# Performance work log

Measured on AMD Instinct MI355X. Metric: run time of the kernel, lower is better.

Reference implementation:

```python
import jax, jax.numpy as jnp
import numpy as np

N_NODES = 100000
N_EDGES = 3200000
F_IN = 128
F_HID = 16
F_OUT = 1


def setup_inputs() -> dict:
    key = jax.random.key(0)
    ks = jax.random.split(key, 8)
    x = jax.random.normal(ks[0], (N_NODES, F_IN), dtype=jnp.float32)
    src = jax.random.randint(ks[1], (N_EDGES,), 0, N_NODES, dtype=jnp.int32)
    dst = jax.random.randint(ks[2], (N_EDGES,), 0, N_NODES, dtype=jnp.int32)
    edge_w = jax.random.uniform(ks[3], (N_EDGES,), dtype=jnp.float32)
    W0 = jax.random.normal(ks[4], (F_IN, F_HID), dtype=jnp.float32) / np.sqrt(F_IN)
    b0 = jnp.zeros((F_HID,), dtype=jnp.float32)
    W1 = jax.random.normal(ks[5], (F_HID, F_OUT), dtype=jnp.float32) / np.sqrt(F_HID)
    b1 = jnp.zeros((F_OUT,), dtype=jnp.float32)
    return {"x": x, "src": src, "dst": dst, "edge_w": edge_w,
            "W0": W0, "b0": b0, "W1": W1, "b1": b1}


def _spmm(src, dst, edge_w, h):
    # sparse A (COO) @ dense h: gather rows at src, weight, scatter-add to dst
    msgs = h[src] * edge_w[:, None]            # [E, F]
    return jax.ops.segment_sum(msgs, dst, num_segments=N_NODES)  # [N, F]


def reference(x, src, dst, edge_w, W0, b0, W1, b1):
    # GCNConv layer 0: relu(A @ (x @ W0) + b0)
    z0 = x @ W0                                 # [N, 16] linear transform first
    h = jax.nn.relu(_spmm(src, dst, edge_w, z0) + b0)
    # (Dropout is identity at inference)
    # GCNConv layer 1: sigmoid(A @ (h @ W1) + b1)
    z1 = h @ W1                                 # [N, 1]
    out = jax.nn.sigmoid(_spmm(src, dst, edge_w, z1) + b1)
    return out
```

## Files before the change

kernel.cpp:

```cpp
#include <hip/hip_runtime.h>

#define N_NODES 100000
#define N_EDGES 3200000
#define F_IN 128
#define F_HID 16

#define BK_LG 7
#define BK_NODES 128
#define NB ((N_NODES + BK_NODES - 1) / BK_NODES)
#define BCAPF 4800
#define CLG 10
#define CNODES 1024
#define NBC ((N_NODES + CNODES - 1) / CNODES)
#define NBC_P 128
#define BCAPC 34816
#define CPB2 9
#define CHUNK 4096
#define BIN_T 512
#define EPT (CHUNK / BIN_T)
#define CUR_STRIDE 16

__device__ __forceinline__ unsigned short f2bf_rne(float f) {
    unsigned u = __float_as_uint(f);
    u += 0x7FFFu + ((u >> 16) & 1u);
    return (unsigned short)(u >> 16);
}

__global__ __launch_bounds__(256) void k_xw0(const float* __restrict__ x,
                                             const float* __restrict__ W0,
                                             unsigned short* __restrict__ z0b, int n) {
    __shared__ float xs[64][F_IN + 1];
    __shared__ float w0s[F_IN * F_HID];
    const int tid = threadIdx.x;
    for (int i = tid; i < F_IN * F_HID; i += 256) w0s[i] = W0[i];
    const int row0 = blockIdx.x * 64;
    for (int i = tid; i < 64 * (F_IN / 4); i += 256) {
        int r  = i / (F_IN / 4);
        int c4 = i % (F_IN / 4);
        float4 v = make_float4(0.f, 0.f, 0.f, 0.f);
        int row = row0 + r;
        if (row < n) v = ((const float4*)(x + (size_t)row * F_IN))[c4];
        xs[r][c4 * 4 + 0] = v.x; xs[r][c4 * 4 + 1] = v.y;
        xs[r][c4 * 4 + 2] = v.z; xs[r][c4 * 4 + 3] = v.w;
    }
    __syncthreads();
    const int r  = tid & 63;
    const int cg = tid >> 6;
    float a0 = 0.f, a1 = 0.f, a2 = 0.f, a3 = 0.f;
    #pragma unroll 8
    for (int k = 0; k < F_IN; ++k) {
        float xv = xs[r][k];
        a0 = fmaf(xv, w0s[k * F_HID + cg * 4 + 0], a0);
        a1 = fmaf(xv, w0s[k * F_HID + cg * 4 + 1], a1);
        a2 = fmaf(xv, w0s[k * F_HID + cg * 4 + 2], a2);
        a3 = fmaf(xv, w0s[k * F_HID + cg * 4 + 3], a3);
    }
    int row = row0 + r;
    if (row < n) {
        ushort4 p = make_ushort4(f2bf_rne(a0), f2bf_rne(a1), f2bf_rne(a2), f2bf_rne(a3));
        *(ushort4*)(z0b + (size_t)row * F_HID + cg * 4) = p;
    }
}

__global__ __launch_bounds__(BIN_T) void k_bin1(const int* __restrict__ src,
                                                const int* __restrict__ dst,
                                                const float* __restrict__ ew,
                                                int* __restrict__ cursorC,
                                                int2* __restrict__ ebinC) {
    __shared__ int cnt[NBC_P], excl[NBC_P], run[NBC_P], gb[NBC_P], alw[NBC_P];
    __shared__ int2 stage[CHUNK];
    __shared__ unsigned char sbid[CHUNK];
    const int tid = threadIdx.x;
    const int e0  = blockIdx.x * CHUNK;
    const int nch = min(CHUNK, N_EDGES - e0);

    for (int i = tid; i < NBC_P; i += BIN_T) cnt[i] = 0;
    __syncthreads();

    int es[EPT], eb[EPT], edl[EPT]; float ww[EPT];
    #pragma unroll
    for (int k = 0; k < EPT; ++k) {
        int idx = k * BIN_T + tid;
        if (idx < nch) {
            int e = e0 + idx;
            int d = dst[e];
            es[k]  = src[e];
            ww[k]  = ew[e];
            eb[k]  = d >> CLG;
            edl[k] = d & (CNODES - 1);
            atomicAdd(&cnt[eb[k]], 1);
        } else {
            eb[k] = -1;
        }
    }
    __syncthreads();

    if (tid < NBC_P) excl[tid] = cnt[tid];
    __syncthreads();
    for (int off = 1; off < NBC_P; off <<= 1) {
        int v = 0;
        if (tid < NBC_P && tid >= off) v = excl[tid - off];
        __syncthreads();
        if (tid < NBC_P && tid >= off) excl[tid] += v;
        __syncthreads();
    }
    if (tid < NBC_P) excl[tid] -= cnt[tid];
    __syncthreads();

    if (tid < NBC) {
        int c = cnt[tid];
        if (c > 0) {
            int old = atomicAdd(&cursorC[tid * CUR_STRIDE], c);
            int a = BCAPC - old;
            a = (a < 0) ? 0 : ((a > c) ? c : a);
            alw[tid] = a;
            gb[tid]  = tid * BCAPC + old;
        } else {
            alw[tid] = 0;
            gb[tid]  = tid * BCAPC;
        }
        run[tid] = 0;
    }
    __syncthreads();

    #pragma unroll
    for (int k = 0; k < EPT; ++k) {
        if (eb[k] >= 0) {
            int b = eb[k];
            int p = excl[b] + atomicAdd(&run[b], 1);
            stage[p] = make_int2(__float_as_int(ww[k]), es[k] | (edl[k] << 17));
            sbid[p]  = (unsigned char)b;
        }
    }
    __syncthreads();

    for (int s = tid; s < nch; s += BIN_T) {
        int b   = sbid[s];
        int off = s - excl[b];
        if (off < alw[b]) ebinC[(size_t)gb[b] + off] = stage[s];
    }
}

__global__ __launch_bounds__(BIN_T) void k_bin2(const int* __restrict__ cursorC,
                                                const int2* __restrict__ ebinC,
                                                int* __restrict__ cursorF,
                                                int2* __restrict__ ebinF) {
    __shared__ int cntw[64], runw[64], base[64];
    __shared__ int totals[8], excl_s[8], gb8[8], alw8[8];
    __shared__ int2 stage[CHUNK];
    __shared__ unsigned char sbid[CHUNK];
    const int tid = threadIdx.x;
    const int wid = tid >> 6;
    const int c   = blockIdx.x / CPB2;
    const int ck  = blockIdx.x % CPB2;
    const int ecnt = min(cursorC[c * CUR_STRIDE], BCAPC);
    const int beg  = ck * CHUNK;
    const int n2   = min(CHUNK, ecnt - beg);
    if (n2 <= 0) return;
    const int2* eC = ebinC + (size_t)c * BCAPC + beg;

    if (tid < 64) { cntw[tid] = 0; runw[tid] = 0; }
    __syncthreads();

    int fid[EPT]; int2 pk[EPT];
    #pragma unroll
    for (int k = 0; k < EPT; ++k) {
        int idx = k * BIN_T + tid;
        if (idx < n2) {
            int2 e = eC[idx];
            int dlc = e.y >> 17;
            int f   = dlc >> BK_LG;
            fid[k]  = f;
            pk[k]   = make_int2(e.x, (e.y & 0x1FFFF) | ((dlc & (BK_NODES - 1)) << 17));
            atomicAdd(&cntw[f * 8 + wid], 1);
        } else {
            fid[k] = -1;
        }
    }
    __syncthreads();

    if (tid < 8) {
        int t = 0;
        #pragma unroll
        for (int w = 0; w < 8; ++w) t += cntw[tid * 8 + w];
        totals[tid] = t;
    }
    __syncthreads();
    if (tid < 8) {
        int e = 0;
        for (int f = 0; f < 8; ++f) if (f < tid) e += totals[f];
        excl_s[tid] = e;
        int t = totals[tid];
        int fb = c * 8 + tid;
        if (t > 0 && fb < NB) {
            int old = atomicAdd(&cursorF[fb * CUR_STRIDE], t);
            int a = BCAPF - old;
            a = (a < 0) ? 0 : ((a > t) ? t : a);
            alw8[tid] = a;
            gb8[tid]  = fb * BCAPF + old;
        } else {
            alw8[tid] = 0;
            gb8[tid]  = 0;
        }
    }
    __syncthreads();
    if (tid < 64) {
        int f = tid >> 3, w = tid & 7;
        int bb = excl_s[f];
        for (int w2 = 0; w2 < 8; ++w2) if (w2 < w) bb += cntw[f * 8 + w2];
        base[tid] = bb;
    }
    __syncthreads();

    #pragma unroll
    for (int k = 0; k < EPT; ++k) {
        if (fid[k] >= 0) {
            int slot = fid[k] * 8 + wid;
            int p = base[slot] + atomicAdd(&runw[slot], 1);
            stage[p] = pk[k];
            sbid[p]  = (unsigned char)fid[k];
        }
    }
    __syncthreads();

    for (int s = tid; s < n2; s += BIN_T) {
        int f   = sbid[s];
        int off = s - excl_s[f];
        if (off < alw8[f]) ebinF[(size_t)gb8[f] + off] = stage[s];
    }
}

__global__ __launch_bounds__(512) void k_sg0(const int* __restrict__ cursorF,
                                             const int2* __restrict__ ebinF,
                                             const unsigned short* __restrict__ z0b,
                                             const float* __restrict__ b0,
                                             const float* __restrict__ W1,
                                             float* __restrict__ z1) {
    __shared__ int2 stage[BCAPF];
    __shared__ unsigned short idx[BCAPF];
    __shared__ int hist[BK_NODES], scn[BK_NODES], run[BK_NODES];
    __shared__ float b0s[16], w1s[16];
    const int tid  = threadIdx.x;
    const int lane = tid & 63, wid = tid >> 6;
    const int b    = blockIdx.x;
    if (tid < 16)       { b0s[tid] = b0[tid]; w1s[tid] = W1[tid]; }
    if (tid < BK_NODES) hist[tid] = 0;
    __syncthreads();

    const int   ecnt = min(cursorF[b * CUR_STRIDE], BCAPF);
    const int2* eb   = ebinF + (size_t)b * BCAPF;
    for (int i = tid; i < ecnt; i += 512) {
        int2 e = eb[i];
        stage[i] = e;
        atomicAdd(&hist[e.y >> 17], 1);
    }
    __syncthreads();

    if (tid < BK_NODES) scn[tid] = hist[tid];
    __syncthreads();
    for (int off = 1; off < BK_NODES; off <<= 1) {
        int v = 0;
        if (tid < BK_NODES && tid >= off) v = scn[tid - off];
        __syncthreads();
        if (tid < BK_NODES && tid >= off) scn[tid] += v;
        __syncthreads();
    }
    if (tid < BK_NODES) { int e = scn[tid] - hist[tid]; scn[tid] = e; run[tid] = 0; }
    __syncthreads();

    for (int i = tid; i < ecnt; i += 512) {
        int dl = stage[i].y >> 17;
        int r  = atomicAdd(&run[dl], 1);
        idx[scn[dl] + r] = (unsigned short)i;
    }
    __syncthreads();

    for (int n = wid; n < BK_NODES; n += 8) {
        const int v = b * BK_NODES + n;
        if (v >= N_NODES) continue;
        const int beg = scn[n], dv = hist[n];
        const int f2  = lane & 7;
        const int g   = lane >> 3;
        float acc0 = 0.f, acc1 = 0.f;
        for (int j = g; j < dv; j += 16) {
            int2 e0 = stage[idx[beg + j]];
            int  j1 = j + 8;
            int2 e1 = (j1 < dv) ? stage[idx[beg + j1]] : stage[0];
            if (j1 >= dv) e1.x = 0;
            unsigned u0 = *(const unsigned*)(z0b + (size_t)(e0.y & 0x1FFFF) * F_HID + f2 * 2);
            unsigned u1 = *(const unsigned*)(z0b + (size_t)(e1.y & 0x1FFFF) * F_HID + f2 * 2);
            float w0 = __int_as_float(e0.x), w1 = __int_as_float(e1.x);
            acc0 = fmaf(__uint_as_float(u0 << 16),         w0, acc0);
            acc1 = fmaf(__uint_as_float(u0 & 0xFFFF0000u), w0, acc1);
            acc0 = fmaf(__uint_as_float(u1 << 16),         w1, acc0);
            acc1 = fmaf(__uint_as_float(u1 & 0xFFFF0000u), w1, acc1);
        }
        acc0 += __shfl_xor(acc0, 8);  acc1 += __shfl_xor(acc1, 8);
        acc0 += __shfl_xor(acc0, 16); acc1 += __shfl_xor(acc1, 16);
        acc0 += __shfl_xor(acc0, 32); acc1 += __shfl_xor(acc1, 32);
        float cc = fmaxf(acc0 + b0s[f2 * 2], 0.f) * w1s[f2 * 2]
                 + fmaxf(acc1 + b0s[f2 * 2 + 1], 0.f) * w1s[f2 * 2 + 1];
        cc += __shfl_xor(cc, 1);
        cc += __shfl_xor(cc, 2);
        cc += __shfl_xor(cc, 4);
        if (lane == 0) z1[v] = cc;
    }
}

__global__ __launch_bounds__(256) void k_g1(const int* __restrict__ cursorF,
                                            const int2* __restrict__ ebinF,
                                            const float* __restrict__ z1,
                                            const float* __restrict__ b1,
                                            float* __restrict__ out) {
    __shared__ float acc[BK_NODES];
    const int tid = threadIdx.x;
    const int b   = blockIdx.x;
    if (tid < BK_NODES) acc[tid] = 0.f;
    __syncthreads();
    const int   ecnt = min(cursorF[b * CUR_STRIDE], BCAPF);
    const int2* eb   = ebinF + (size_t)b * BCAPF;
    for (int i = tid; i < ecnt; i += 512) {
        int2 e0 = eb[i];
        int  i1 = i + 256;
        int2 e1 = (i1 < ecnt) ? eb[i1] : make_int2(0, 0);
        float m0 = z1[e0.y & 0x1FFFF] * __int_as_float(e0.x);
        float m1 = z1[e1.y & 0x1FFFF] * __int_as_float(e1.x);
        atomicAdd(&acc[e0.y >> 17], m0);
        if (i1 < ecnt) atomicAdd(&acc[e1.y >> 17], m1);
    }
    __syncthreads();
    if (tid < BK_NODES) {
        int v = b * BK_NODES + tid;
        if (v < N_NODES) out[v] = 1.f / (1.f + expf(-(acc[tid] + b1[0])));
    }
}

extern "C" void kernel_launch(void* const* d_in, const int* in_sizes, int n_in,
                              void* d_out, int out_size, void* d_ws, size_t ws_size,
                              hipStream_t stream) {
    const float* x   = (const float*)d_in[0];
    const int*   src = (const int*)d_in[1];
    const int*   dst = (const int*)d_in[2];
    const float* ew  = (const float*)d_in[3];
    const float* W0  = (const float*)d_in[4];
    const float* b0  = (const float*)d_in[5];
    const float* W1  = (const float*)d_in[6];
    const float* b1  = (const float*)d_in[7];
    float* out = (float*)d_out;

    unsigned short* z0b = (unsigned short*)d_ws;
    float* z1      = (float*)(z0b + (size_t)N_NODES * F_HID);
    int*   cursorC = (int*)(z1 + N_NODES);
    int*   cursorF = cursorC + NBC * CUR_STRIDE;
    int2*  ebinC   = (int2*)(cursorF + NB * CUR_STRIDE);
    int2*  ebinF   = ebinC + (size_t)NBC * BCAPC;

    hipMemsetAsync(cursorC, 0,
                   (size_t)(NBC + NB) * CUR_STRIDE * sizeof(int), stream);

    k_bin1<<<(N_EDGES + CHUNK - 1) / CHUNK, BIN_T, 0, stream>>>(src, dst, ew,
                                                                cursorC, ebinC);
    k_xw0 <<<(N_NODES + 63) / 64, 256, 0, stream>>>(x, W0, z0b, N_NODES);
    k_bin2<<<NBC * CPB2, BIN_T, 0, stream>>>(cursorC, ebinC, cursorF, ebinF);
    k_sg0 <<<NB, 512, 0, stream>>>(cursorF, ebinF, z0b, b0, W1, z1);
    k_g1  <<<NB, 256, 0, stream>>>(cursorF, ebinF, z1, b1, out);
}
```

Measured before the change: 148.2 us.

## Fuse x@W0 with first binning pass and precompute per-node degrees

Merges the x@W0 transform and the first coarse edge-binning pass into one kernel whose even blocks do the matmul and odd blocks bin edges, so the two independent stages run concurrently. The second binning pass now also counts per-destination degrees in shared memory and atomically adds them to a global degree array. The aggregation kernel then reads that array instead of rebuilding its own histogram, and scatters edges directly into a sorted shared buffer rather than using an index indirection. Block prefix scans switch to wavefront shuffles and BCAPF shrinks slightly. The cost is extra global atomics for degrees and a larger memset.

```diff
diff --git a/kernel.cpp b/kernel.cpp
--- a/kernel.cpp
+++ b/kernel.cpp
@@ -8,16 +8,17 @@
 #define BK_LG 7
 #define BK_NODES 128
 #define NB ((N_NODES + BK_NODES - 1) / BK_NODES)
-#define BCAPF 4800
+#define BCAPF 4736
 #define CLG 10
 #define CNODES 1024
 #define NBC ((N_NODES + CNODES - 1) / CNODES)
 #define NBC_P 128
 #define BCAPC 34816
 #define CPB2 9
-#define CHUNK 4096
-#define BIN_T 512
-#define EPT (CHUNK / BIN_T)
+#define CHUNK2 4096
+#define CHUNK1 2048
+#define NCH1 ((N_EDGES + CHUNK1 - 1) / CHUNK1)
+#define NXB ((N_NODES + 63) / 64)
 #define CUR_STRIDE 16
 
 __device__ __forceinline__ unsigned short f2bf_rne(float f) {
@@ -26,146 +27,172 @@
     return (unsigned short)(u >> 16);
 }
 
-__global__ __launch_bounds__(256) void k_xw0(const float* __restrict__ x,
+__global__ __launch_bounds__(256) void k_pre(const float* __restrict__ x,
                                              const float* __restrict__ W0,
-                                             unsigned short* __restrict__ z0b, int n) {
-    __shared__ float xs[64][F_IN + 1];
-    __shared__ float w0s[F_IN * F_HID];
+                                             unsigned short* __restrict__ z0b,
+                                             const int* __restrict__ src,
+                                             const int* __restrict__ dst,
+                                             const float* __restrict__ ew,
+                                             int* __restrict__ cursorC,
+                                             int2* __restrict__ ebinC) {
+    __shared__ __align__(16) char smem[41216];
     const int tid = threadIdx.x;
-    for (int i = tid; i < F_IN * F_HID; i += 256) w0s[i] = W0[i];
-    const int row0 = blockIdx.x * 64;
-    for (int i = tid; i < 64 * (F_IN / 4); i += 256) {
-        int r  = i / (F_IN / 4);
-        int c4 = i % (F_IN / 4);
-        float4 v = make_float4(0.f, 0.f, 0.f, 0.f);
+
+    if ((blockIdx.x & 1) == 0) {
+        const int xb = blockIdx.x >> 1;
+        if (xb >= NXB) return;
+        float* xs  = (float*)smem;
+        float* w0s = (float*)(smem + 33024);
+        for (int i = tid; i < F_IN * F_HID; i += 256) w0s[i] = W0[i];
+        const int row0 = xb * 64;
+        for (int i = tid; i < 64 * (F_IN / 4); i += 256) {
+            int r  = i / (F_IN / 4);
+            int c4 = i % (F_IN / 4);
+            float4 v = make_float4(0.f, 0.f, 0.f, 0.f);
+            int row = row0 + r;
+            if (row < N_NODES) v = ((const float4*)(x + (size_t)row * F_IN))[c4];
+            xs[r * 129 + c4 * 4 + 0] = v.x; xs[r * 129 + c4 * 4 + 1] = v.y;
+            xs[r * 129 + c4 * 4 + 2] = v.z; xs[r * 129 + c4 * 4 + 3] = v.w;
+        }
+        __syncthreads();
+        const int r  = tid & 63;
+        const int cg = tid >> 6;
+        float a0 = 0.f, a1 = 0.f, a2 = 0.f, a3 = 0.f;
+        #pragma unroll 8
+        for (int k = 0; k < F_IN; ++k) {
+            float xv = xs[r * 129 + k];
+            a0 = fmaf(xv, w0s[k * F_HID + cg * 4 + 0], a0);
+            a1 = fmaf(xv, w0s[k * F_HID + cg * 4 + 1], a1);
+            a2 = fmaf(xv, w0s[k * F_HID + cg * 4 + 2], a2);
+            a3 = fmaf(xv, w0s[k * F_HID + cg * 4 + 3], a3);
+        }
         int row = row0 + r;
-        if (row < n) v = ((const float4*)(x + (size_t)row * F_IN))[c4];
-        xs[r][c4 * 4 + 0] = v.x; xs[r][c4 * 4 + 1] = v.y;
-        xs[r][c4 * 4 + 2] = v.z; xs[r][c4 * 4 + 3] = v.w;
-    }
-    __syncthreads();
-    const int r  = tid & 63;
-    const int cg = tid >> 6;
-    float a0 = 0.f, a1 = 0.f, a2 = 0.f, a3 = 0.f;
-    #pragma unroll 8
-    for (int k = 0; k < F_IN; ++k) {
-        float xv = xs[r][k];
-        a0 = fmaf(xv, w0s[k * F_HID + cg * 4 + 0], a0);
-        a1 = fmaf(xv, w0s[k * F_HID + cg * 4 + 1], a1);
-        a2 = fmaf(xv, w0s[k * F_HID + cg * 4 + 2], a2);
-        a3 = fmaf(xv, w0s[k * F_HID + cg * 4 + 3], a3);
-    }
-    int row = row0 + r;
-    if (row < n) {
-        ushort4 p = make_ushort4(f2bf_rne(a0), f2bf_rne(a1), f2bf_rne(a2), f2bf_rne(a3));
-        *(ushort4*)(z0b + (size_t)row * F_HID + cg * 4) = p;
-    }
-}
-
-__global__ __launch_bounds__(BIN_T) void k_bin1(const int* __restrict__ src,
-                                                const int* __restrict__ dst,
-                                                const float* __restrict__ ew,
-                                                int* __restrict__ cursorC,
-                                                int2* __restrict__ ebinC) {
-    __shared__ int cnt[NBC_P], excl[NBC_P], run[NBC_P], gb[NBC_P], alw[NBC_P];
-    __shared__ int2 stage[CHUNK];
-    __shared__ unsigned char sbid[CHUNK];
-    const int tid = threadIdx.x;
-    const int e0  = blockIdx.x * CHUNK;
-    const int nch = min(CHUNK, N_EDGES - e0);
-
-    for (int i = tid; i < NBC_P; i += BIN_T) cnt[i] = 0;
-    __syncthreads();
-
-    int es[EPT], eb[EPT], edl[EPT]; float ww[EPT];
-    #pragma unroll
-    for (int k = 0; k < EPT; ++k) {
-        int idx = k * BIN_T + tid;
-        if (idx < nch) {
-            int e = e0 + idx;
-            int d = dst[e];
-            es[k]  = src[e];
-            ww[k]  = ew[e];
-            eb[k]  = d >> CLG;
-            edl[k] = d & (CNODES - 1);
-            atomicAdd(&cnt[eb[k]], 1);
-        } else {
-            eb[k] = -1;
-        }
-    }
-    __syncthreads();
-
-    if (tid < NBC_P) excl[tid] = cnt[tid];
-    __syncthreads();
-    for (int off = 1; off < NBC_P; off <<= 1) {
-        int v = 0;
-        if (tid < NBC_P && tid >= off) v = excl[tid - off];
-        __syncthreads();
-        if (tid < NBC_P && tid >= off) excl[tid] += v;
-        __syncthreads();
-    }
-    if (tid < NBC_P) excl[tid] -= cnt[tid];
-    __syncthreads();
-
-    if (tid < NBC) {
-        int c = cnt[tid];
-        if (c > 0) {
-            int old = atomicAdd(&cursorC[tid * CUR_STRIDE], c);
-            int a = BCAPC - old;
-            a = (a < 0) ? 0 : ((a > c) ? c : a);
-            alw[tid] = a;
-            gb[tid]  = tid * BCAPC + old;
-        } else {
-            alw[tid] = 0;
-            gb[tid]  = tid * BCAPC;
-        }
-        run[tid] = 0;
-    }
-    __syncthreads();
-
-    #pragma unroll
-    for (int k = 0; k < EPT; ++k) {
-        if (eb[k] >= 0) {
-            int b = eb[k];
-            int p = excl[b] + atomicAdd(&run[b], 1);
-            stage[p] = make_int2(__float_as_int(ww[k]), es[k] | (edl[k] << 17));
-            sbid[p]  = (unsigned char)b;
-        }
-    }
-    __syncthreads();
-
-    for (int s = tid; s < nch; s += BIN_T) {
-        int b   = sbid[s];
-        int off = s - excl[b];
-        if (off < alw[b]) ebinC[(size_t)gb[b] + off] = stage[s];
-    }
-}
-
-__global__ __launch_bounds__(BIN_T) void k_bin2(const int* __restrict__ cursorC,
-                                                const int2* __restrict__ ebinC,
-                                                int* __restrict__ cursorF,
-                                                int2* __restrict__ ebinF) {
+        if (row < N_NODES) {
+            ushort4 p = make_ushort4(f2bf_rne(a0), f2bf_rne(a1),
+                                     f2bf_rne(a2), f2bf_rne(a3));
+            *(ushort4*)(z0b + (size_t)row * F_HID + cg * 4) = p;
+        }
+    } else {
+        const int ch = blockIdx.x >> 1;
+        if (ch >= NCH1) return;
+        int2* stage = (int2*)smem;
+        unsigned char* sbid = (unsigned char*)(smem + 16384);
+        int* cnt  = (int*)(smem + 18432);
+        int* excl = (int*)(smem + 18944);
+        int* run  = (int*)(smem + 19456);
+        int* gb   = (int*)(smem + 19968);
+        int* alw  = (int*)(smem + 20480);
+        int* wtot = (int*)(smem + 20992);
+        const int e0  = ch * CHUNK1;
+        const int nch = min(CHUNK1, N_EDGES - e0);
+
+        for (int i = tid; i < NBC_P; i += 256) cnt[i] = 0;
+        __syncthreads();
+
+        const int EPT1 = CHUNK1 / 256;
+        int es[8], eb[8], edl[8]; float ww[8];
+        #pragma unroll
+        for (int k = 0; k < EPT1; ++k) {
+            int idx = k * 256 + tid;
+            if (idx < nch) {
+                int e = e0 + idx;
+                int d = dst[e];
+                es[k]  = src[e];
+                ww[k]  = ew[e];
+                eb[k]  = d >> CLG;
+                edl[k] = d & (CNODES - 1);
+                atomicAdd(&cnt[eb[k]], 1);
+            } else {
+                eb[k] = -1;
+            }
+        }
+        __syncthreads();
+
+        {
+            const int lane = tid & 63;
+            int inc = 0, dv_ = 0;
+            if (tid < NBC_P) {
+                dv_ = cnt[tid];
+                inc = dv_;
+                #pragma unroll
+                for (int off = 1; off < 64; off <<= 1) {
+                    int t = __shfl_up(inc, off);
+                    if (lane >= off) inc += t;
+                }
+                if (lane == 63) wtot[tid >> 6] = inc;
+            }
+            __syncthreads();
+            if (tid < NBC_P) {
+                int base = (tid >= 64) ? wtot[0] : 0;
+                excl[tid] = base + inc - dv_;
+            }
+        }
+        __syncthreads();
+
+        if (tid < NBC) {
+            int c = cnt[tid];
+            if (c > 0) {
+                int old = atomicAdd(&cursorC[tid * CUR_STRIDE], c);
+                int a = BCAPC - old;
+                a = (a < 0) ? 0 : ((a > c) ? c : a);
+                alw[tid] = a;
+                gb[tid]  = tid * BCAPC + old;
+            } else {
+                alw[tid] = 0;
+                gb[tid]  = tid * BCAPC;
+            }
+            run[tid] = 0;
+        }
+        __syncthreads();
+
+        #pragma unroll
+        for (int k = 0; k < EPT1; ++k) {
+            if (eb[k] >= 0) {
+                int b = eb[k];
+                int p = excl[b] + atomicAdd(&run[b], 1);
+                stage[p] = make_int2(__float_as_int(ww[k]), es[k] | (edl[k] << 17));
+                sbid[p]  = (unsigned char)b;
+            }
+        }
+        __syncthreads();
+
+        for (int s = tid; s < nch; s += 256) {
+            int b   = sbid[s];
+            int off = s - excl[b];
+            if (off < alw[b]) ebinC[(size_t)gb[b] + off] = stage[s];
+        }
+    }
+}
+
+__global__ __launch_bounds__(512) void k_bin2(const int* __restrict__ cursorC,
+                                              const int2* __restrict__ ebinC,
+                                              int* __restrict__ cursorF,
+                                              int2* __restrict__ ebinF,
+                                              int* __restrict__ deg) {
     __shared__ int cntw[64], runw[64], base[64];
     __shared__ int totals[8], excl_s[8], gb8[8], alw8[8];
-    __shared__ int2 stage[CHUNK];
-    __shared__ unsigned char sbid[CHUNK];
+    __shared__ int dcnt[CNODES];
+    __shared__ int2 stage[CHUNK2];
+    __shared__ unsigned char sbid[CHUNK2];
     const int tid = threadIdx.x;
     const int wid = tid >> 6;
     const int c   = blockIdx.x / CPB2;
     const int ck  = blockIdx.x % CPB2;
     const int ecnt = min(cursorC[c * CUR_STRIDE], BCAPC);
-    const int beg  = ck * CHUNK;
-    const int n2   = min(CHUNK, ecnt - beg);
+    const int beg  = ck * CHUNK2;
+    const int n2   = min(CHUNK2, ecnt - beg);
     if (n2 <= 0) return;
     const int2* eC = ebinC + (size_t)c * BCAPC + beg;
 
     if (tid < 64) { cntw[tid] = 0; runw[tid] = 0; }
-    __syncthreads();
-
-    int fid[EPT]; int2 pk[EPT];
+    for (int i = tid; i < CNODES; i += 512) dcnt[i] = 0;
+    __syncthreads();
+
+    const int EPT2 = CHUNK2 / 512;
+    int fid[8]; int2 pk[8];
     #pragma unroll
-    for (int k = 0; k < EPT; ++k) {
-        int idx = k * BIN_T + tid;
+    for (int k = 0; k < EPT2; ++k) {
+        int idx = k * 512 + tid;
         if (idx < n2) {
             int2 e = eC[idx];
             int dlc = e.y >> 17;
@@ -173,6 +200,7 @@
             fid[k]  = f;
             pk[k]   = make_int2(e.x, (e.y & 0x1FFFF) | ((dlc & (BK_NODES - 1)) << 17));
             atomicAdd(&cntw[f * 8 + wid], 1);
+            atomicAdd(&dcnt[dlc], 1);
         } else {
             fid[k] = -1;
         }
@@ -213,7 +241,7 @@
     __syncthreads();
 
     #pragma unroll
-    for (int k = 0; k < EPT; ++k) {
+    for (int k = 0; k < EPT2; ++k) {
         if (fid[k] >= 0) {
             int slot = fid[k] * 8 + wid;
             int p = base[slot] + atomicAdd(&runw[slot], 1);
@@ -223,70 +251,79 @@
     }
     __syncthreads();
 
-    for (int s = tid; s < n2; s += BIN_T) {
+    for (int s = tid; s < n2; s += 512) {
         int f   = sbid[s];
         int off = s - excl_s[f];
         if (off < alw8[f]) ebinF[(size_t)gb8[f] + off] = stage[s];
     }
-}
-
-__global__ __launch_bounds__(512) void k_sg0(const int* __restrict__ cursorF,
+
+    for (int i = tid; i < CNODES; i += 512) {
+        int d = dcnt[i];
+        int v = c * CNODES + i;
+        if (d > 0 && v < N_NODES) atomicAdd(&deg[v], d);
+    }
+}
+
+__global__ __launch_bounds__(512) void k_sg0(const int* __restrict__ deg,
                                              const int2* __restrict__ ebinF,
                                              const unsigned short* __restrict__ z0b,
                                              const float* __restrict__ b0,
                                              const float* __restrict__ W1,
                                              float* __restrict__ z1) {
-    __shared__ int2 stage[BCAPF];
-    __shared__ unsigned short idx[BCAPF];
-    __shared__ int hist[BK_NODES], scn[BK_NODES], run[BK_NODES];
+    __shared__ int2 sorted[BCAPF];
+    __shared__ int scn[BK_NODES], dg[BK_NODES], run[BK_NODES];
+    __shared__ int wtot[2], ecnt_s;
     __shared__ float b0s[16], w1s[16];
     const int tid  = threadIdx.x;
     const int lane = tid & 63, wid = tid >> 6;
     const int b    = blockIdx.x;
-    if (tid < 16)       { b0s[tid] = b0[tid]; w1s[tid] = W1[tid]; }
-    if (tid < BK_NODES) hist[tid] = 0;
-    __syncthreads();
-
-    const int   ecnt = min(cursorF[b * CUR_STRIDE], BCAPF);
-    const int2* eb   = ebinF + (size_t)b * BCAPF;
+    if (tid < 16) { b0s[tid] = b0[tid]; w1s[tid] = W1[tid]; }
+
+    int inc = 0, d_ = 0;
+    if (tid < BK_NODES) {
+        int v = b * BK_NODES + tid;
+        d_ = (v < N_NODES) ? deg[v] : 0;
+        dg[tid]  = d_;
+        run[tid] = 0;
+        inc = d_;
+        #pragma unroll
+        for (int off = 1; off < 64; off <<= 1) {
+            int t = __shfl_up(inc, off);
+            if (lane >= off) inc += t;
+        }
+        if (lane == 63) wtot[tid >> 6] = inc;
+    }
+    __syncthreads();
+    if (tid < BK_NODES) {
+        int base = (tid >= 64) ? wtot[0] : 0;
+        scn[tid] = base + inc - d_;
+        if (tid == BK_NODES - 1) ecnt_s = min(base + inc, BCAPF);
+    }
+    __syncthreads();
+
+    const int ecnt = ecnt_s;
+    const int2* eb = ebinF + (size_t)b * BCAPF;
     for (int i = tid; i < ecnt; i += 512) {
-        int2 e = eb[i];
-        stage[i] = e;
-        atomicAdd(&hist[e.y >> 17], 1);
-    }
-    __syncthreads();
-
-    if (tid < BK_NODES) scn[tid] = hist[tid];
-    __syncthreads();
-    for (int off = 1; off < BK_NODES; off <<= 1) {
-        int v = 0;
-        if (tid < BK_NODES && tid >= off) v = scn[tid - off];
-        __syncthreads();
-        if (tid < BK_NODES && tid >= off) scn[tid] += v;
-        __syncthreads();
-    }
-    if (tid < BK_NODES) { int e = scn[tid] - hist[tid]; scn[tid] = e; run[tid] = 0; }
-    __syncthreads();
-
-    for (int i = tid; i < ecnt; i += 512) {
-        int dl = stage[i].y >> 17;
-        int r  = atomicAdd(&run[dl], 1);
-        idx[scn[dl] + r] = (unsigned short)i;
+        int2 e  = eb[i];
+        int  dl = e.y >> 17;
+        int  p  = scn[dl] + atomicAdd(&run[dl], 1);
+        if (p < BCAPF) sorted[p] = e;
     }
     __syncthreads();
 
     for (int n = wid; n < BK_NODES; n += 8) {
         const int v = b * BK_NODES + n;
         if (v >= N_NODES) continue;
-        const int beg = scn[n], dv = hist[n];
+        const int beg = scn[n];
+        const int end = min(beg + dg[n], BCAPF);
+        const int dv  = end - beg;
         const int f2  = lane & 7;
         const int g   = lane >> 3;
         float acc0 = 0.f, acc1 = 0.f;
         for (int j = g; j < dv; j += 16) {
-            int2 e0 = stage[idx[beg + j]];
+            int2 e0 = sorted[beg + j];
             int  j1 = j + 8;
-            int2 e1 = (j1 < dv) ? stage[idx[beg + j1]] : stage[0];
-            if (j1 >= dv) e1.x = 0;
+            int2 e1 = (j1 < dv) ? sorted[beg + j1] : make_int2(0, 0);
             unsigned u0 = *(const unsigned*)(z0b + (size_t)(e0.y & 0x1FFFF) * F_HID + f2 * 2);
             unsigned u1 = *(const unsigned*)(z0b + (size_t)(e1.y & 0x1FFFF) * F_HID + f2 * 2);
             float w0 = __int_as_float(e0.x), w1 = __int_as_float(e1.x);
@@ -350,18 +387,18 @@
 
     unsigned short* z0b = (unsigned short*)d_ws;
     float* z1      = (float*)(z0b + (size_t)N_NODES * F_HID);
-    int*   cursorC = (int*)(z1 + N_NODES);
+    int*   deg     = (int*)(z1 + N_NODES);
+    int*   cursorC = deg + N_NODES;
     int*   cursorF = cursorC + NBC * CUR_STRIDE;
     int2*  ebinC   = (int2*)(cursorF + NB * CUR_STRIDE);
     int2*  ebinF   = ebinC + (size_t)NBC * BCAPC;
 
-    hipMemsetAsync(cursorC, 0,
-                   (size_t)(NBC + NB) * CUR_STRIDE * sizeof(int), stream);
-
-    k_bin1<<<(N_EDGES + CHUNK - 1) / CHUNK, BIN_T, 0, stream>>>(src, dst, ew,
-                                                                cursorC, ebinC);
-    k_xw0 <<<(N_NODES + 63) / 64, 256, 0, stream>>>(x, W0, z0b, N_NODES);
-    k_bin2<<<NBC * CPB2, BIN_T, 0, stream>>>(cursorC, ebinC, cursorF, ebinF);
-    k_sg0 <<<NB, 512, 0, stream>>>(cursorF, ebinF, z0b, b0, W1, z1);
+    hipMemsetAsync(deg, 0,
+                   ((size_t)N_NODES + (size_t)(NBC + NB) * CUR_STRIDE) * sizeof(int),
+                   stream);
+
+    k_pre <<<2 * NCH1, 256, 0, stream>>>(x, W0, z0b, src, dst, ew, cursorC, ebinC);
+    k_bin2<<<NBC * CPB2, 512, 0, stream>>>(cursorC, ebinC, cursorF, ebinF, deg);
+    k_sg0 <<<NB, 512, 0, stream>>>(deg, ebinF, z0b, b0, W1, z1);
     k_g1  <<<NB, 256, 0, stream>>>(cursorF, ebinF, z1, b1, out);
 }
```

After: 130.4 us. -12.0%, faster.
